# Kernel tuning notes

Hardware: AMD Instinct MI355X
Metric: run time of the kernel (lower is better)

## Reference

```python
import jax, jax.numpy as jnp
import numpy as np

SPIKE_PROB = 0.3


def setup_inputs() -> dict:
    key = jax.random.key(0)
    T, B, C, H, W = 4, 32, 128, 56, 56
    u = jax.random.uniform(key, (T, B, C, H, W), dtype=jnp.float32)
    spikes = (u < SPIKE_PROB).astype(jnp.float32)  # binary spike trains
    return {"spikes": spikes, "TIME": T}


def reference(spikes, TIME):
    # spikes: [TIME, B, C, H, W] binary spike tensor, one slice per forward call.
    # Replicates Sparsity_Checker over a full TIME window:
    #   spike_collector accumulates spikes over t;
    #   sparsity_ratio = mean over t of per-step zero fraction (divided by TIME at t==TIME);
    #   temp_sparsity_ratio_of_collector = zero fraction of final collector;
    #   unique(return_counts) on integer-valued collector == bincount over 0..TIME.
    total = spikes[0].size  # elements per timestep

    # per-step zero fractions, then average over TIME (matches /= self.TIME)
    per_step_zero = jnp.sum(spikes == 0, axis=tuple(range(1, spikes.ndim)))  # [TIME]
    sparsity_ratio = jnp.sum(per_step_zero.astype(jnp.float32)) / (total * TIME)

    # final accumulated collector (state after the last forward call)
    collector = jnp.sum(spikes, axis=0)  # [B, C, H, W], integer-valued 0..TIME

    coll_zero_frac = jnp.sum(collector == 0).astype(jnp.float32) / total

    # histogram of collector values: unique_vals are 0..TIME, counts via bincount
    unique_counts = jnp.bincount(collector.astype(jnp.int32).ravel(), length=TIME + 1)

    # module returns the input spike unchanged; stats are side outputs
    return spikes, sparsity_ratio, coll_zero_frac, unique_counts
```

## Files before the change

kernel.cpp:

```cpp
#include <hip/hip_runtime.h>


constexpr int T_STEPS = 4;

__global__ __launch_bounds__(256) void spike_stats_kernel(
    const float4* __restrict__ in, float4* __restrict__ out,
    unsigned int* __restrict__ hist, int nvec)
{
    __shared__ unsigned int lhist[5];
    if (threadIdx.x < 5) lhist[threadIdx.x] = 0u;
    __syncthreads();

    unsigned long long packed = 0ull;

    const int stride = gridDim.x * blockDim.x;
    for (int v = blockIdx.x * blockDim.x + threadIdx.x; v < nvec; v += stride) {
        float4 a0 = in[0 * nvec + v];
        float4 a1 = in[1 * nvec + v];
        float4 a2 = in[2 * nvec + v];
        float4 a3 = in[3 * nvec + v];
        out[0 * nvec + v] = a0;
        out[1 * nvec + v] = a1;
        out[2 * nvec + v] = a2;
        out[3 * nvec + v] = a3;
        int cx = (int)(a0.x + a1.x + a2.x + a3.x);
        int cy = (int)(a0.y + a1.y + a2.y + a3.y);
        int cz = (int)(a0.z + a1.z + a2.z + a3.z);
        int cw = (int)(a0.w + a1.w + a2.w + a3.w);
        packed += (1ull << (cx * 12)) + (1ull << (cy * 12))
                + (1ull << (cz * 12)) + (1ull << (cw * 12));
    }

#pragma unroll
    for (int off = 32; off > 0; off >>= 1)
        packed += __shfl_down(packed, off, 64);

    if ((threadIdx.x & 63) == 0) {
#pragma unroll
        for (int k = 0; k < 5; ++k)
            atomicAdd(&lhist[k], (unsigned int)((packed >> (12 * k)) & 0xFFFull));
    }
    __syncthreads();

    if (threadIdx.x < 5)
        atomicAdd(&hist[threadIdx.x], lhist[threadIdx.x]);
}

__global__ void finalize_kernel(const unsigned int* __restrict__ hist,
                                float* __restrict__ tail, double total)
{
    if (threadIdx.x == 0 && blockIdx.x == 0) {
        double spikes_sum = 0.0;
#pragma unroll
        for (int k = 0; k < 5; ++k)
            spikes_sum += (double)k * (double)hist[k];
        double denom = total * (double)T_STEPS;
        tail[0] = (float)((denom - spikes_sum) / denom);
        tail[1] = (float)((double)hist[0] / total);
#pragma unroll
        for (int k = 0; k < 5; ++k)
            tail[2 + k] = (float)hist[k];
    }
}

extern "C" void kernel_launch(void* const* d_in, const int* in_sizes, int n_in,
                              void* d_out, int out_size, void* d_ws, size_t ws_size,
                              hipStream_t stream)
{
    const float* spikes = (const float*)d_in[0];
    float* out = (float*)d_out;

    const long n = (long)in_sizes[0];
    const long per_t = n / T_STEPS;
    const int nvec = (int)(per_t / 4);

    unsigned int* hist = (unsigned int*)d_ws;
    hipMemsetAsync(d_ws, 0, 5 * sizeof(unsigned int), stream);

    spike_stats_kernel<<<dim3(1024), dim3(256), 0, stream>>>(
        (const float4*)spikes, (float4*)out, hist, nvec);

    finalize_kernel<<<dim3(1), dim3(64), 0, stream>>>(hist, out + n, (double)per_t);
}
```

Baseline: 349.5 us.

## Fuse finalize into stats kernel via last-block counter and use nontemporal I/O

Removes the separate finalize kernel launch: each block increments a done counter after its histogram atomics, and the last block computes the sparsity ratios and counts. Global loads and stores switch to nontemporal builtins to avoid cache pollution for the streaming copy, and the grid doubles to 2048 blocks. This saves one launch gap at the cost of an extra fence and atomic per block, and nontemporal hints may or may not help HBM streaming on this part.

```diff
diff --git a/kernel.cpp b/kernel.cpp
--- a/kernel.cpp
+++ b/kernel.cpp
@@ -3,30 +3,48 @@
 
 constexpr int T_STEPS = 4;
 
+typedef float f4 __attribute__((ext_vector_type(4)));
+
 __global__ __launch_bounds__(256) void spike_stats_kernel(
-    const float4* __restrict__ in, float4* __restrict__ out,
-    unsigned int* __restrict__ hist, int nvec)
+    const f4* __restrict__ in, f4* __restrict__ out,
+    unsigned int* __restrict__ ws, float* __restrict__ tail,
+    int nvec, double total)
 {
+    unsigned int* hist = ws;
+    unsigned int* done = ws + 5;
+
     __shared__ unsigned int lhist[5];
+    __shared__ bool amLast;
     if (threadIdx.x < 5) lhist[threadIdx.x] = 0u;
+    if (threadIdx.x == 0) amLast = false;
     __syncthreads();
+
+    const f4* __restrict__ i0 = in;
+    const f4* __restrict__ i1 = in + (size_t)nvec;
+    const f4* __restrict__ i2 = in + 2 * (size_t)nvec;
+    const f4* __restrict__ i3 = in + 3 * (size_t)nvec;
+    f4* __restrict__ o0 = out;
+    f4* __restrict__ o1 = out + (size_t)nvec;
+    f4* __restrict__ o2 = out + 2 * (size_t)nvec;
+    f4* __restrict__ o3 = out + 3 * (size_t)nvec;
 
     unsigned long long packed = 0ull;
 
     const int stride = gridDim.x * blockDim.x;
     for (int v = blockIdx.x * blockDim.x + threadIdx.x; v < nvec; v += stride) {
-        float4 a0 = in[0 * nvec + v];
-        float4 a1 = in[1 * nvec + v];
-        float4 a2 = in[2 * nvec + v];
-        float4 a3 = in[3 * nvec + v];
-        out[0 * nvec + v] = a0;
-        out[1 * nvec + v] = a1;
-        out[2 * nvec + v] = a2;
-        out[3 * nvec + v] = a3;
-        int cx = (int)(a0.x + a1.x + a2.x + a3.x);
-        int cy = (int)(a0.y + a1.y + a2.y + a3.y);
-        int cz = (int)(a0.z + a1.z + a2.z + a3.z);
-        int cw = (int)(a0.w + a1.w + a2.w + a3.w);
+        f4 a0 = __builtin_nontemporal_load(i0 + v);
+        f4 a1 = __builtin_nontemporal_load(i1 + v);
+        f4 a2 = __builtin_nontemporal_load(i2 + v);
+        f4 a3 = __builtin_nontemporal_load(i3 + v);
+        __builtin_nontemporal_store(a0, o0 + v);
+        __builtin_nontemporal_store(a1, o1 + v);
+        __builtin_nontemporal_store(a2, o2 + v);
+        __builtin_nontemporal_store(a3, o3 + v);
+        f4 s = a0 + a1 + a2 + a3;
+        int cx = (int)s[0];
+        int cy = (int)s[1];
+        int cz = (int)s[2];
+        int cw = (int)s[3];
         packed += (1ull << (cx * 12)) + (1ull << (cy * 12))
                 + (1ull << (cz * 12)) + (1ull << (cw * 12));
     }
@@ -44,22 +62,30 @@
 
     if (threadIdx.x < 5)
         atomicAdd(&hist[threadIdx.x], lhist[threadIdx.x]);
-}
 
-__global__ void finalize_kernel(const unsigned int* __restrict__ hist,
-                                float* __restrict__ tail, double total)
-{
-    if (threadIdx.x == 0 && blockIdx.x == 0) {
+    __threadfence();
+    if (threadIdx.x == 0) {
+        unsigned int prev = __hip_atomic_fetch_add(
+            done, 1u, __ATOMIC_ACQ_REL, __HIP_MEMORY_SCOPE_AGENT);
+        amLast = (prev == gridDim.x - 1);
+    }
+    __syncthreads();
+
+    if (amLast && threadIdx.x == 0) {
+        unsigned int h[5];
         double spikes_sum = 0.0;
 #pragma unroll
-        for (int k = 0; k < 5; ++k)
-            spikes_sum += (double)k * (double)hist[k];
+        for (int k = 0; k < 5; ++k) {
+            h[k] = __hip_atomic_load(&hist[k], __ATOMIC_RELAXED,
+                                     __HIP_MEMORY_SCOPE_AGENT);
+            spikes_sum += (double)k * (double)h[k];
+        }
         double denom = total * (double)T_STEPS;
         tail[0] = (float)((denom - spikes_sum) / denom);
-        tail[1] = (float)((double)hist[0] / total);
+        tail[1] = (float)((double)h[0] / total);
 #pragma unroll
         for (int k = 0; k < 5; ++k)
-            tail[2 + k] = (float)hist[k];
+            tail[2 + k] = (float)h[k];
     }
 }
 
@@ -74,11 +100,9 @@
     const long per_t = n / T_STEPS;
     const int nvec = (int)(per_t / 4);
 
-    unsigned int* hist = (unsigned int*)d_ws;
-    hipMemsetAsync(d_ws, 0, 5 * sizeof(unsigned int), stream);
+    unsigned int* ws = (unsigned int*)d_ws;
+    hipMemsetAsync(d_ws, 0, 6 * sizeof(unsigned int), stream);
 
-    spike_stats_kernel<<<dim3(1024), dim3(256), 0, stream>>>(
-        (const float4*)spikes, (float4*)out, hist, nvec);
-
-    finalize_kernel<<<dim3(1), dim3(64), 0, stream>>>(hist, out + n, (double)per_t);
+    spike_stats_kernel<<<dim3(2048), dim3(256), 0, stream>>>(
+        (const f4*)spikes, (f4*)out, ws, out + n, nvec, (double)per_t);
 }
```

Result: slower. 766.7 us (+119.4%).
